# Performance work log

Measured on AMD Instinct MI355X. Metric: run time of the kernel, lower is better.

Reference implementation:

```python
import jax, jax.numpy as jnp
import numpy as np

VOCAB, EMB, T = 10000, 100, 80
UNITS, BATCH = 256, 4096


def setup_inputs() -> dict:
    key = jax.random.key(0)
    ks = jax.random.split(key, 8)
    s = lambda k, shape, scale: jax.random.normal(k, shape, jnp.float32) * scale
    return {
        "inputs": jax.random.randint(ks[0], (BATCH, T), 0, VOCAB, dtype=jnp.int32),
        "emb": s(ks[1], (VOCAB, EMB), 0.05),
        "W1": s(ks[2], (EMB, UNITS), 1.0 / np.sqrt(EMB)),
        "U1": s(ks[3], (UNITS, UNITS), 1.0 / np.sqrt(UNITS)),
        "b1": jnp.zeros((UNITS,), jnp.float32),
        "W2": s(ks[4], (UNITS, UNITS), 1.0 / np.sqrt(UNITS)),
        "U2": s(ks[5], (UNITS, UNITS), 1.0 / np.sqrt(UNITS)),
        "b2": jnp.zeros((UNITS,), jnp.float32),
        "Wd": s(ks[6], (UNITS, 1), 1.0 / np.sqrt(UNITS)),
        "bd": jnp.zeros((1,), jnp.float32),
    }


def _simple_rnn(xs, W, U, b, return_sequences):
    # xs: [B, T, D]; h_t = tanh(x_t @ W + h_{t-1} @ U + b) (Keras SimpleRNN, eval mode)
    B = xs.shape[0]
    H = U.shape[0]
    xproj = jnp.einsum('btd,dh->bth', xs, W) + b  # precompute input projection
    h0 = jnp.zeros((B, H), xs.dtype)

    def step(h, xp):
        h = jnp.tanh(xp + h @ U)
        return h, h

    hT, hs = jax.lax.scan(step, h0, jnp.swapaxes(xproj, 0, 1))  # scan over time
    return jnp.swapaxes(hs, 0, 1) if return_sequences else hT


def reference(inputs, emb, W1, U1, b1, W2, U2, b2, Wd, bd):
    x = emb[inputs]                                   # [B, T, EMB]
    x = _simple_rnn(x, W1, U1, b1, return_sequences=True)   # [B, T, UNITS]
    x = _simple_rnn(x, W2, U2, b2, return_sequences=False)  # [B, UNITS]
    s = x @ Wd + bd  # computed in original but unused in returned value
    del s
    return jax.nn.sigmoid(x)                          # original returns sigmoid(x), not sigmoid(s)
```

## Files before the change

kernel.cpp:

```cpp
#include <hip/hip_runtime.h>

#define BATCH 4096
#define TLEN  80
#define EMBD  100
#define UNITS 256

typedef _Float16 f16;
typedef __attribute__((ext_vector_type(8))) _Float16 h8;
typedef __attribute__((ext_vector_type(4))) float f32x4;

__device__ __forceinline__ float fast_tanh(float x) {
  float ax = __builtin_fabsf(x);
  float e  = __expf(-2.f * ax);
  float r  = (1.f - e) * __builtin_amdgcn_rcpf(1.f + e);
  return __builtin_copysignf(r, x);
}
__device__ __forceinline__ float fast_sigmoid(float x) {
  return __builtin_amdgcn_rcpf(1.f + __expf(-x));
}

__device__ __forceinline__ void block_sync_lds() {
  asm volatile("s_waitcnt lgkmcnt(0)\n\ts_barrier" ::: "memory");
}

#define KT_ALL 28
#define OFF_P1 ((size_t)0)
#define P1_BYTES ((size_t)10000 * UNITS * 2)
#define OFF_WF  P1_BYTES
#define WF_BYTES ((size_t)KT_ALL * 16 * 64 * 8 * 2)
#define WS_NEED (OFF_WF + WF_BYTES)

__device__ __forceinline__ size_t fidx(int ktg, int nt, int lane) {
  return (((size_t)ktg * 16 + nt) * 64 + lane) * 8;
}

__global__ __launch_bounds__(256) void k_split_w16(
    const float* __restrict__ W1, const float* __restrict__ U1,
    const float* __restrict__ W2, const float* __restrict__ U2,
    f16* __restrict__ wf)
{
  int gid = blockIdx.x * 256 + threadIdx.x;
  if (gid >= KT_ALL * 16 * 64) return;
  int lane = gid & 63, nt = (gid >> 6) & 15, ktg = gid >> 10;
  const float* M; int Kact, ktl;
  if (ktg < 4)       { M = W1; Kact = EMBD;  ktl = ktg;      }
  else if (ktg < 12) { M = U1; Kact = UNITS; ktl = ktg - 4;  }
  else if (ktg < 20) { M = W2; Kact = UNITS; ktl = ktg - 12; }
  else               { M = U2; Kact = UNITS; ktl = ktg - 20; }
  int n = nt * 16 + (lane & 15);
  int kb = ktl * 32 + (lane >> 4) * 8;
  size_t base = fidx(ktg, nt, lane);
#pragma unroll
  for (int j = 0; j < 8; ++j) {
    int k = kb + j;
    wf[base + j] = (f16)((k < Kact) ? M[(size_t)k * UNITS + n] : 0.f);
  }
}

__global__ __launch_bounds__(256) void k_p1(
    const float* __restrict__ emb, const float* __restrict__ W1,
    const float* __restrict__ b1, f16* __restrict__ p1t)
{
  __shared__ float er[16][EMBD];
  const int v0 = blockIdx.x * 16;
  for (int i = threadIdx.x; i < 16 * EMBD; i += 256) {
    int vv = i / EMBD, kk = i - vv * EMBD;
    er[vv][kk] = emb[(size_t)(v0 + vv) * EMBD + kk];
  }
  __syncthreads();
  const int n = threadIdx.x;
  float acc[16];
  const float bb = b1[n];
#pragma unroll
  for (int vv = 0; vv < 16; ++vv) acc[vv] = bb;
  for (int k = 0; k < EMBD; ++k) {
    float w = W1[(size_t)k * UNITS + n];
#pragma unroll
    for (int vv = 0; vv < 16; ++vv) acc[vv] += er[vv][k] * w;
  }
#pragma unroll
  for (int vv = 0; vv < 16; ++vv)
    p1t[(size_t)(v0 + vv) * UNITS + n] = (f16)acc[vv];
}

#define MFMA16(A, B, C) __builtin_amdgcn_mfma_f32_16x16x32_f16(A, B, C, 0, 0, 0)

__device__ __forceinline__ void store_frag1(f16* __restrict__ f, int col, int row, float v) {
  int a = (col >> 5) * 512 + (((col >> 3) & 3) * 16 + row) * 8 + (col & 7);
  f[a] = (f16)v;
}

#define P1S 264

__global__ __launch_bounds__(512, 2)
__attribute__((amdgpu_waves_per_eu(2, 2)))
void rnn_wsB(
    const int* __restrict__ idx, const f16* __restrict__ p1t,
    const f16* __restrict__ wf, const float* __restrict__ b2,
    float* __restrict__ out)
{
  __shared__ __align__(16) f16 f1[2][4096];
  __shared__ __align__(16) f16 f2[2][4096];
  __shared__ __align__(16) f16 p1s[2][16 * P1S];
  extern __shared__ f16 u2s[];

  const int tid  = threadIdx.x;
  const int lane = tid & 63;
  const int w    = tid >> 6;
  const int m    = lane & 15;
  const int q    = lane >> 4;
  const int b0   = blockIdx.x * 16;
  const int c0   = (2 * w) * 16 + m;
  const int c1   = (2 * w + 1) * 16 + m;

  const float b2a = b2[c0], b2b = b2[c1];

  const int srow = tid >> 5, spart = tid & 31;
  const int* tokp = idx + (size_t)(b0 + srow) * TLEN;
  const f16* p1g  = p1t + spart * 8;

  for (int d = tid; d < 4096; d += 512) {
    int l = d & 63, g = d >> 6, no = g >> 3, kt = g & 7;
    *(h8*)&u2s[(size_t)d * 8] = *(const h8*)(wf + fidx(20 + kt, 2 * no + 1, l));
  }

  h8 Bu1a[8], Bu1b[8], Bw2a[8], Bw2b[8], Bu2a[8];
#pragma unroll
  for (int kt = 0; kt < 8; ++kt) {
    Bu1a[kt] = *(const h8*)(wf + fidx(4 + kt, 2 * w, lane));
    Bu1b[kt] = *(const h8*)(wf + fidx(4 + kt, 2 * w + 1, lane));
    Bw2a[kt] = *(const h8*)(wf + fidx(12 + kt, 2 * w, lane));
    Bw2b[kt] = *(const h8*)(wf + fidx(12 + kt, 2 * w + 1, lane));
    Bu2a[kt] = *(const h8*)(wf + fidx(20 + kt, 2 * w, lane));
  }
#pragma unroll
  for (int kt = 0; kt < 8; ++kt) {
    asm volatile("" : "+v"(Bu1a[kt])); asm volatile("" : "+v"(Bu1b[kt]));
    asm volatile("" : "+v"(Bw2a[kt])); asm volatile("" : "+v"(Bw2b[kt]));
    asm volatile("" : "+v"(Bu2a[kt]));
  }

  for (int i = tid; i < 4096; i += 512) f2[0][i] = (f16)0.f;

#pragma unroll
  for (int r = 0; r < 4; ++r) {
    int row = q * 4 + r;
    int tk = idx[(size_t)(b0 + row) * TLEN + 0];
    const f16* pr = p1t + (size_t)tk * UNITS;
    store_frag1(f1[0], c0, row, fast_tanh((float)pr[c0]));
    store_frag1(f1[0], c1, row, fast_tanh((float)pr[c1]));
  }

  {
    int tk1 = tokp[1];
    h8 v = *(const h8*)(p1g + (size_t)tk1 * UNITS);
    *(h8*)&p1s[1][srow * P1S + spart * 8] = v;
  }
  int tkn = tokp[2];
  __syncthreads();

#define RNN_STEP(RD, WR, STAGE, TKI)                                         \
  {                                                                          \
    h8 p1v;                                                                  \
    if (STAGE) p1v = *(const h8*)(p1g + (size_t)tkn * UNITS);                \
    tkn = tokp[TKI];                                                         \
    f32x4 x0, x1;                                                            \
    _Pragma("unroll")                                                        \
    for (int r = 0; r < 4; ++r) {                                            \
      int row = q * 4 + r;                                                   \
      x0[r] = (float)p1s[WR][row * P1S + c0];                                \
      x1[r] = (float)p1s[WR][row * P1S + c1];                                \
    }                                                                        \
    f32x4 yA0 = (f32x4){b2a, b2a, b2a, b2a};                                 \
    f32x4 yA1 = (f32x4){b2b, b2b, b2b, b2b};                                 \
    f32x4 yB0 = (f32x4){0.f, 0.f, 0.f, 0.f};                                 \
    f32x4 yB1 = (f32x4){0.f, 0.f, 0.f, 0.f};                                 \
    _Pragma("unroll")                                                        \
    for (int kt = 0; kt < 8; ++kt) {                                         \
      h8 a1 = *(const h8*)&f1[RD][kt * 512 + lane * 8];                      \
      h8 a2 = *(const h8*)&f2[RD][kt * 512 + lane * 8];                      \
      h8 ub = *(const h8*)&u2s[((w * 8 + kt) * 64 + lane) * 8];              \
      x0  = MFMA16(a1, Bu1a[kt], x0);                                        \
      x1  = MFMA16(a1, Bu1b[kt], x1);                                        \
      yA0 = MFMA16(a1, Bw2a[kt], yA0);                                       \
      yA1 = MFMA16(a1, Bw2b[kt], yA1);                                       \
      yB0 = MFMA16(a2, Bu2a[kt], yB0);                                       \
      yB1 = MFMA16(a2, ub,       yB1);                                       \
    }                                                                        \
    _Pragma("unroll")                                                        \
    for (int r = 0; r < 4; ++r) {                                            \
      int row = q * 4 + r;                                                   \
      store_frag1(f1[WR], c0, row, fast_tanh(x0[r]));                        \
      store_frag1(f1[WR], c1, row, fast_tanh(x1[r]));                        \
      store_frag1(f2[WR], c0, row, fast_tanh(yA0[r] + yB0[r]));              \
      store_frag1(f2[WR], c1, row, fast_tanh(yA1[r] + yB1[r]));              \
    }                                                                        \
    if (STAGE) *(h8*)&p1s[RD][srow * P1S + spart * 8] = p1v;                 \
    block_sync_lds();                                                        \
  }

  for (int i = 1; i < TLEN - 1; i += 2) {
    int t2 = i + 3 < TLEN - 1 ? i + 3 : TLEN - 1;
    RNN_STEP(0, 1, true, i + 2);
    RNN_STEP(1, 0, true, t2);
  }
  RNN_STEP(0, 1, false, TLEN - 1);
#undef RNN_STEP

  {
    f32x4 yA0 = (f32x4){b2a, b2a, b2a, b2a};
    f32x4 yA1 = (f32x4){b2b, b2b, b2b, b2b};
    f32x4 yB0 = (f32x4){0.f, 0.f, 0.f, 0.f};
    f32x4 yB1 = (f32x4){0.f, 0.f, 0.f, 0.f};
#pragma unroll
    for (int kt = 0; kt < 8; ++kt) {
      h8 a1 = *(const h8*)&f1[1][kt * 512 + lane * 8];
      h8 a2 = *(const h8*)&f2[1][kt * 512 + lane * 8];
      h8 ub = *(const h8*)&u2s[((w * 8 + kt) * 64 + lane) * 8];
      yA0 = MFMA16(a1, Bw2a[kt], yA0);
      yA1 = MFMA16(a1, Bw2b[kt], yA1);
      yB0 = MFMA16(a2, Bu2a[kt], yB0);
      yB1 = MFMA16(a2, ub,       yB1);
    }
#pragma unroll
    for (int r = 0; r < 4; ++r) {
      int row = q * 4 + r;
      out[(size_t)(b0 + row) * UNITS + c0] = fast_sigmoid(fast_tanh(yA0[r] + yB0[r]));
      out[(size_t)(b0 + row) * UNITS + c1] = fast_sigmoid(fast_tanh(yA1[r] + yB1[r]));
    }
  }
}

extern "C" void kernel_launch(void* const* d_in, const int* in_sizes, int n_in,
                              void* d_out, int out_size, void* d_ws, size_t ws_size,
                              hipStream_t stream)
{
  const int*   idx = (const int*)d_in[0];
  const float* emb = (const float*)d_in[1];
  const float* W1  = (const float*)d_in[2];
  const float* U1  = (const float*)d_in[3];
  const float* b1  = (const float*)d_in[4];
  const float* W2  = (const float*)d_in[5];
  const float* U2  = (const float*)d_in[6];
  const float* b2  = (const float*)d_in[7];
  float* out = (float*)d_out;

  static bool attr_done = false;
  if (!attr_done) {
    (void)hipFuncSetAttribute((const void*)rnn_wsB,
                              hipFuncAttributeMaxDynamicSharedMemorySize,
                              65536);
    attr_done = true;
  }

  f16* p1t = (f16*)((char*)d_ws + OFF_P1);
  f16* wf  = (f16*)((char*)d_ws + OFF_WF);
  k_p1<<<10000 / 16, 256, 0, stream>>>(emb, W1, b1, p1t);
  k_split_w16<<<(KT_ALL * 16 * 64 + 255) / 256, 256, 0, stream>>>(W1, U1, W2, U2, wf);
  rnn_wsB<<<BATCH / 16, 512, 65536, stream>>>(idx, p1t, wf, b2, out);
}
```

Before: 222.5 us.

## Stream U2 second-half fragments from global/L2 each step instead of LDS

Drops the 64KB dynamic LDS copy of the second half of U2 and instead reloads those B-fragments from global memory (L2-resident) at the start of every timestep. The MFMA loop is split so the layer-1 products run first, giving the global loads time to land before the U2 products need them. This cuts LDS footprint and LDS read traffic, which may allow more blocks per CU. In exchange it adds per-step global/L2 traffic and load latency on the recurrence's critical path.

```diff
diff --git a/kernel.cpp b/kernel.cpp
--- a/kernel.cpp
+++ b/kernel.cpp
@@ -94,7 +94,7 @@
 
 __global__ __launch_bounds__(512, 2)
 __attribute__((amdgpu_waves_per_eu(2, 2)))
-void rnn_wsB(
+void rnn_wsC(
     const int* __restrict__ idx, const f16* __restrict__ p1t,
     const f16* __restrict__ wf, const float* __restrict__ b2,
     float* __restrict__ out)
@@ -102,7 +102,6 @@
   __shared__ __align__(16) f16 f1[2][4096];
   __shared__ __align__(16) f16 f2[2][4096];
   __shared__ __align__(16) f16 p1s[2][16 * P1S];
-  extern __shared__ f16 u2s[];
 
   const int tid  = threadIdx.x;
   const int lane = tid & 63;
@@ -117,12 +116,8 @@
 
   const int srow = tid >> 5, spart = tid & 31;
   const int* tokp = idx + (size_t)(b0 + srow) * TLEN;
-  const f16* p1g  = p1t + spart * 8;
-
-  for (int d = tid; d < 4096; d += 512) {
-    int l = d & 63, g = d >> 6, no = g >> 3, kt = g & 7;
-    *(h8*)&u2s[(size_t)d * 8] = *(const h8*)(wf + fidx(20 + kt, 2 * no + 1, l));
-  }
+  const f16* __restrict__ p1g = p1t + spart * 8;
+  const f16* __restrict__ u2g = wf + fidx(20, 2 * w + 1, lane);
 
   h8 Bu1a[8], Bu1b[8], Bw2a[8], Bw2b[8], Bu2a[8];
 #pragma unroll
@@ -161,6 +156,10 @@
 
 #define RNN_STEP(RD, WR, STAGE, TKI)                                         \
   {                                                                          \
+    h8 ub[8];                                                                \
+    _Pragma("unroll")                                                        \
+    for (int kt = 0; kt < 8; ++kt)                                           \
+      ub[kt] = *(const h8*)(u2g + kt * 8192);                                \
     h8 p1v;                                                                  \
     if (STAGE) p1v = *(const h8*)(p1g + (size_t)tkn * UNITS);                \
     tkn = tokp[TKI];                                                         \
@@ -178,14 +177,16 @@
     _Pragma("unroll")                                                        \
     for (int kt = 0; kt < 8; ++kt) {                                         \
       h8 a1 = *(const h8*)&f1[RD][kt * 512 + lane * 8];                      \
-      h8 a2 = *(const h8*)&f2[RD][kt * 512 + lane * 8];                      \
-      h8 ub = *(const h8*)&u2s[((w * 8 + kt) * 64 + lane) * 8];              \
       x0  = MFMA16(a1, Bu1a[kt], x0);                                        \
       x1  = MFMA16(a1, Bu1b[kt], x1);                                        \
       yA0 = MFMA16(a1, Bw2a[kt], yA0);                                       \
       yA1 = MFMA16(a1, Bw2b[kt], yA1);                                       \
+    }                                                                        \
+    _Pragma("unroll")                                                        \
+    for (int kt = 0; kt < 8; ++kt) {                                         \
+      h8 a2 = *(const h8*)&f2[RD][kt * 512 + lane * 8];                      \
       yB0 = MFMA16(a2, Bu2a[kt], yB0);                                       \
-      yB1 = MFMA16(a2, ub,       yB1);                                       \
+      yB1 = MFMA16(a2, ub[kt],   yB1);                                       \
     }                                                                        \
     _Pragma("unroll")                                                        \
     for (int r = 0; r < 4; ++r) {                                            \
@@ -216,7 +217,7 @@
     for (int kt = 0; kt < 8; ++kt) {
       h8 a1 = *(const h8*)&f1[1][kt * 512 + lane * 8];
       h8 a2 = *(const h8*)&f2[1][kt * 512 + lane * 8];
-      h8 ub = *(const h8*)&u2s[((w * 8 + kt) * 64 + lane) * 8];
+      h8 ub = *(const h8*)(u2g + kt * 8192);
       yA0 = MFMA16(a1, Bw2a[kt], yA0);
       yA1 = MFMA16(a1, Bw2b[kt], yA1);
       yB0 = MFMA16(a2, Bu2a[kt], yB0);
@@ -245,17 +246,9 @@
   const float* b2  = (const float*)d_in[7];
   float* out = (float*)d_out;
 
-  static bool attr_done = false;
-  if (!attr_done) {
-    (void)hipFuncSetAttribute((const void*)rnn_wsB,
-                              hipFuncAttributeMaxDynamicSharedMemorySize,
-                              65536);
-    attr_done = true;
-  }
-
   f16* p1t = (f16*)((char*)d_ws + OFF_P1);
   f16* wf  = (f16*)((char*)d_ws + OFF_WF);
   k_p1<<<10000 / 16, 256, 0, stream>>>(emb, W1, b1, p1t);
   k_split_w16<<<(KT_ALL * 16 * 64 + 255) / 256, 256, 0, stream>>>(W1, U1, W2, U2, wf);
-  rnn_wsB<<<BATCH / 16, 512, 65536, stream>>>(idx, p1t, wf, b2, out);
-}
+  rnn_wsC<<<BATCH / 16, 512, 0, stream>>>(idx, p1t, wf, b2, out);
+}
```

New measurement: 310.0 us. 1.39x slower.
